# Optimization experiments

Hardware: AMD Instinct MI355X
Metric: run time of the kernel (lower is better)

## Reference

```python
import jax, jax.numpy as jnp
import numpy as np

B, L_ENC, L_DEC, PRED_LEN = 16, 720, 144, 96
D_MODEL, N_HEADS, D_FF, M_FEAT = 512, 8, 2048, 256
ENC_IN, DEC_IN, C_OUT, MARK = 7, 7, 7, 4
E_LAYERS = 2
DH = D_MODEL // N_HEADS


def _orf(m, d, seed):
    # Gaussian orthogonal random features (FAVOR+), scaling=0 (chi-norm rows).
    rng = np.random.default_rng(seed)
    blocks = [np.linalg.qr(rng.standard_normal((d, d)))[0].T for _ in range(m // d)]
    mat = np.concatenate(blocks, 0)  # [m, d]
    mult = np.linalg.norm(rng.standard_normal((m, d)), axis=1)
    return jnp.asarray(mult[:, None] * mat, dtype=jnp.float32)

PROJ_ENC = [_orf(M_FEAT, DH, s) for s in range(E_LAYERS)]
PROJ_DEC_SELF = _orf(M_FEAT, DH, 10)
PROJ_DEC_CROSS = _orf(M_FEAT, DH, 11)


def _pos_emb(n, d):
    pos = np.arange(n, dtype=np.float32)[:, None]
    div = np.exp(np.arange(0, d, 2, dtype=np.float32) * (-np.log(10000.0) / d))
    pe = np.zeros((n, d), dtype=np.float32)
    pe[:, 0::2] = np.sin(pos * div)
    pe[:, 1::2] = np.cos(pos * div)
    return jnp.asarray(pe)

PE_ENC = _pos_emb(L_ENC, D_MODEL)
PE_DEC = _pos_emb(L_DEC, D_MODEL)


def layer_norm(x, g, b):
    mu = x.mean(-1, keepdims=True)
    var = ((x - mu) ** 2).mean(-1, keepdims=True)
    return (x - mu) / jnp.sqrt(var + 1e-5) * g + b


def feature_map(x, proj, is_query):
    # FAVOR+ positive softmax kernel. x: [b,h,n,dh], proj: [m,dh]
    norm = DH ** -0.25
    xd = jnp.einsum('bhnd,md->bhnm', x * norm, proj)
    diag = (x ** 2).sum(-1) * (0.5 * norm * norm)  # [b,h,n]
    if is_query:
        stab = jax.lax.stop_gradient(xd.max(axis=-1, keepdims=True))
    else:
        stab = jax.lax.stop_gradient(xd.max(axis=(-1, -2), keepdims=True))
    return (M_FEAT ** -0.5) * (jnp.exp(xd - diag[..., None] - stab) + 1e-4)


def noncausal_attn(q, k, v):
    kv = jnp.einsum('bhnm,bhnd->bhmd', k, v)
    d_inv = 1.0 / jnp.einsum('bhnm,bhm->bhn', q, k.sum(2))
    return jnp.einsum('bhnm,bhmd,bhn->bhnd', q, kv, d_inv)


def causal_attn(q, k, v):
    # prefix-sum linear attention; carry S [b,h,m,dh], s [b,h,m]
    b, h, n, m = q.shape
    dh = v.shape[-1]

    def step(carry, qkv):
        S, s = carry
        qn, kn, vn = qkv
        S = S + kn[..., None] * vn[..., None, :]
        s = s + kn
        num = jnp.einsum('bhm,bhmd->bhd', qn, S)
        den = jnp.einsum('bhm,bhm->bh', qn, s)
        return (S, s), num / (den[..., None] + 1e-6)

    init = (jnp.zeros((b, h, m, dh), q.dtype), jnp.zeros((b, h, m), q.dtype))
    _, out = jax.lax.scan(step, init, (jnp.moveaxis(q, 2, 0), jnp.moveaxis(k, 2, 0), jnp.moveaxis(v, 2, 0)))
    return jnp.moveaxis(out, 0, 2)


def attention(x, ctx, Wq, Wk, Wv, Wo, bo, proj, causal):
    b, n, _ = x.shape
    nc = ctx.shape[1]
    q = (x @ Wq).reshape(b, n, N_HEADS, DH).transpose(0, 2, 1, 3)
    k = (ctx @ Wk).reshape(b, nc, N_HEADS, DH).transpose(0, 2, 1, 3)
    v = (ctx @ Wv).reshape(b, nc, N_HEADS, DH).transpose(0, 2, 1, 3)
    qp = feature_map(q, proj, True)
    kp = feature_map(k, proj, False)
    o = causal_attn(qp, kp, v) if causal else noncausal_attn(qp, kp, v)
    o = o.transpose(0, 2, 1, 3).reshape(b, n, D_MODEL)
    return o @ Wo + bo


def embed(x, mark, conv_w, time_w, pe):
    # TokenEmbedding: circular conv1d k=3 (no bias) + fixed sinusoidal PE + timeF linear
    xp = jnp.concatenate([x[:, -1:], x, x[:, :1]], axis=1)
    tok = (jnp.einsum('blc,cd->bld', xp[:, :-2], conv_w[0])
           + jnp.einsum('blc,cd->bld', xp[:, 1:-1], conv_w[1])
           + jnp.einsum('blc,cd->bld', xp[:, 2:], conv_w[2]))
    return tok + pe[None] + mark @ time_w


def _forward(x_enc, x_mark_enc, x_dec, x_mark_dec,
             emb_conv_enc, emb_time_enc, emb_conv_dec, emb_time_dec,
             enc_Wq, enc_Wk, enc_Wv, enc_Wo, enc_bo,
             enc_ff1, enc_b1, enc_ff2, enc_b2, enc_ln_g, enc_ln_b, enc_fg, enc_fb,
             dec_sWq, dec_sWk, dec_sWv, dec_sWo, dec_sbo,
             dec_cWq, dec_cWk, dec_cWv, dec_cWo, dec_cbo,
             dec_ff1, dec_b1, dec_ff2, dec_b2, dec_ln_g, dec_ln_b, dec_fg, dec_fb,
             proj_w, proj_b):
    gelu = lambda t: jax.nn.gelu(t, approximate=False)
    # RevIN-style instance normalization (means detached, as in the torch code)
    means = jax.lax.stop_gradient(x_enc.mean(1, keepdims=True))
    xc = x_enc - means
    stdev = jnp.sqrt(xc.var(1, keepdims=True) + 1e-5)
    xe = xc / stdev

    enc = embed(xe, x_mark_enc, emb_conv_enc, emb_time_enc, PE_ENC)
    for i in range(E_LAYERS):
        a = attention(enc, enc, enc_Wq[i], enc_Wk[i], enc_Wv[i], enc_Wo[i], enc_bo[i], PROJ_ENC[i], False)
        x1 = layer_norm(enc + a, enc_ln_g[i, 0], enc_ln_b[i, 0])
        y = gelu(x1 @ enc_ff1[i] + enc_b1[i]) @ enc_ff2[i] + enc_b2[i]
        enc = layer_norm(x1 + y, enc_ln_g[i, 1], enc_ln_b[i, 1])
    enc = layer_norm(enc, enc_fg, enc_fb)

    dec = embed(x_dec, x_mark_dec, emb_conv_dec, emb_time_dec, PE_DEC)
    a = attention(dec, dec, dec_sWq, dec_sWk, dec_sWv, dec_sWo, dec_sbo, PROJ_DEC_SELF, True)
    x1 = layer_norm(dec + a, dec_ln_g[0], dec_ln_b[0])
    c = attention(x1, enc, dec_cWq, dec_cWk, dec_cWv, dec_cWo, dec_cbo, PROJ_DEC_CROSS, False)
    x2 = layer_norm(x1 + c, dec_ln_g[1], dec_ln_b[1])
    y = gelu(x2 @ dec_ff1 + dec_b1) @ dec_ff2 + dec_b2
    dec = layer_norm(x2 + y, dec_ln_g[2], dec_ln_b[2])
    dec = layer_norm(dec, dec_fg, dec_fb)
    out = dec @ proj_w + proj_b  # [B, L_DEC, C_OUT]

    out = out * stdev[:, 0][:, None, :] + means[:, 0][:, None, :]
    return out[:, -PRED_LEN:, :]


def setup_inputs():
    ks = iter(jax.random.split(jax.random.key(0), 48))

    def rn(shape, scale=1.0):
        return jax.random.normal(next(ks), shape, dtype=jnp.float32) * scale

    w = 0.02
    E, D, F = E_LAYERS, D_MODEL, D_FF
    return {
        'x_enc': rn((B, L_ENC, ENC_IN)),
        'x_mark_enc': rn((B, L_ENC, MARK)),
        'x_dec': rn((B, L_DEC, DEC_IN)),
        'x_mark_dec': rn((B, L_DEC, MARK)),
        'emb_conv_enc': rn((3, ENC_IN, D), 0.1),
        'emb_time_enc': rn((MARK, D), w),
        'emb_conv_dec': rn((3, DEC_IN, D), 0.1),
        'emb_time_dec': rn((MARK, D), w),
        'enc_Wq': rn((E, D, D), w), 'enc_Wk': rn((E, D, D), w),
        'enc_Wv': rn((E, D, D), w), 'enc_Wo': rn((E, D, D), w),
        'enc_bo': jnp.zeros((E, D), jnp.float32),
        'enc_ff1': rn((E, D, F), w), 'enc_b1': jnp.zeros((E, F), jnp.float32),
        'enc_ff2': rn((E, F, D), w), 'enc_b2': jnp.zeros((E, D), jnp.float32),
        'enc_ln_g': jnp.ones((E, 2, D), jnp.float32), 'enc_ln_b': jnp.zeros((E, 2, D), jnp.float32),
        'enc_fg': jnp.ones((D,), jnp.float32), 'enc_fb': jnp.zeros((D,), jnp.float32),
        'dec_sWq': rn((D, D), w), 'dec_sWk': rn((D, D), w), 'dec_sWv': rn((D, D), w), 'dec_sWo': rn((D, D), w),
        'dec_sbo': jnp.zeros((D,), jnp.float32),
        'dec_cWq': rn((D, D), w), 'dec_cWk': rn((D, D), w), 'dec_cWv': rn((D, D), w), 'dec_cWo': rn((D, D), w),
        'dec_cbo': jnp.zeros((D,), jnp.float32),
        'dec_ff1': rn((D, F), w), 'dec_b1': jnp.zeros((F,), jnp.float32),
        'dec_ff2': rn((F, D), w), 'dec_b2': jnp.zeros((D,), jnp.float32),
        'dec_ln_g': jnp.ones((3, D), jnp.float32), 'dec_ln_b': jnp.zeros((3, D), jnp.float32),
        'dec_fg': jnp.ones((D,), jnp.float32), 'dec_fb': jnp.zeros((D,), jnp.float32),
        'proj_w': rn((D, C_OUT), w), 'proj_b': jnp.zeros((C_OUT,), jnp.float32),
    }


def reference(x_enc, x_mark_enc, x_dec, x_mark_dec,
              emb_conv_enc, emb_time_enc, emb_conv_dec, emb_time_dec,
              enc_Wq, enc_Wk, enc_Wv, enc_Wo, enc_bo,
              enc_ff1, enc_b1, enc_ff2, enc_b2, enc_ln_g, enc_ln_b, enc_fg, enc_fb,
              dec_sWq, dec_sWk, dec_sWv, dec_sWo, dec_sbo,
              dec_cWq, dec_cWk, dec_cWv, dec_cWo, dec_cbo,
              dec_ff1, dec_b1, dec_ff2, dec_b2, dec_ln_g, dec_ln_b, dec_fg, dec_fb,
              proj_w, proj_b):
    return _forward(x_enc, x_mark_enc, x_dec, x_mark_dec,
                    emb_conv_enc, emb_time_enc, emb_conv_dec, emb_time_dec,
                    enc_Wq, enc_Wk, enc_Wv, enc_Wo, enc_bo,
                    enc_ff1, enc_b1, enc_ff2, enc_b2, enc_ln_g, enc_ln_b, enc_fg, enc_fb,
                    dec_sWq, dec_sWk, dec_sWv, dec_sWo, dec_sbo,
                    dec_cWq, dec_cWk, dec_cWv, dec_cWo, dec_cbo,
                    dec_ff1, dec_b1, dec_ff2, dec_b2, dec_ln_g, dec_ln_b, dec_fg, dec_fb,
                    proj_w, proj_b)
```

## Files before the change

### kernel.cpp

```cpp
#include <hip/hip_runtime.h>
#include <math.h>
#include <string.h>

#define BB    16
#define LEc   720
#define LDc   144
#define PREDc 96
#define DMc   512
#define NHc   8
#define DHc   64
#define MFc   256
#define FFc   2048
#define NEc   (BB*LEc)
#define NDc   (BB*LDc)
#define BHc   (BB*NHc)
#define KSn   ((size_t)BHc*MFc)

typedef unsigned int u32;
typedef unsigned short u16;
typedef unsigned long long u64;
typedef unsigned __int128 u128;

typedef short bfx8 __attribute__((ext_vector_type(8)));
typedef float fx4  __attribute__((ext_vector_type(4)));
// ... 193 lines not shown
                                             int K, int N){
  __shared__ float t[32][33];
  int kb = blockIdx.x*32, nb = blockIdx.y*32;
  int tx = threadIdx.x & 31, ty = threadIdx.x >> 5;
  #pragma unroll
  for (int p=0;p<4;p++)
    t[ty + p*8][tx] = W[(size_t)(kb + ty + p*8)*N + nb + tx];
  __syncthreads();
  #pragma unroll
  for (int p=0;p<4;p++)
    WT[(size_t)(nb + ty + p*8)*K + kb + tx] = f2bf(t[tx][ty + p*8]);
}

__global__ __launch_bounds__(64) void k_meanstd(const float* __restrict__ x,
                                                float* __restrict__ means, float* __restrict__ stdev){
  int bc = blockIdx.x; int b = bc/7, c = bc%7;
  int t = threadIdx.x;
  float s=0;
  for (int l=t; l<LEc; l+=64) s += x[((size_t)b*LEc+l)*7 + c];
  for (int o=32;o;o>>=1) s += __shfl_down(s,o);
  s = __shfl(s,0);
  float mu = s / (float)LEc;
  float v=0;
  for (int l=t; l<LEc; l+=64){ float d = x[((size_t)b*LEc+l)*7+c]-mu; v += d*d; }
  for (int o=32;o;o>>=1) v += __shfl_down(v,o);
  if (t==0){ means[bc]=mu; stdev[bc]=sqrtf(v/(float)LEc + 1e-5f); }
}

__global__ __launch_bounds__(256) void k_embed(const float* __restrict__ x, const float* __restrict__ mark,
    const float* __restrict__ convw, const float* __restrict__ timew, const float* __restrict__ pe,
    const float* __restrict__ means, const float* __restrict__ stdev,
    int L, int donorm, float* __restrict__ outp)
{
  size_t idx = (size_t)blockIdx.x*256 + threadIdx.x;
  size_t total = (size_t)BB*L*DMc;
  if (idx >= total) return;
  int d = (int)(idx % DMc); size_t bl = idx / DMc; int l = (int)(bl % L); int b = (int)(bl / L);
  int lm = (l==0)? L-1 : l-1;
  int lp = (l==L-1)? 0 : l+1;
  float acc = pe[(size_t)l*DMc + d];
  const float* xb = x + (size_t)b*L*7;
  #pragma unroll
  for (int c=0;c<7;c++){
    float v0 = xb[(size_t)lm*7+c], v1 = xb[(size_t)l*7+c], v2 = xb[(size_t)lp*7+c];
    if (donorm){
      float mu = means[b*7+c], sd = stdev[b*7+c];
      v0=(v0-mu)/sd; v1=(v1-mu)/sd; v2=(v2-mu)/sd;
    }
    acc += v0*convw[(0*7+c)*DMc+d] + v1*convw[(1*7+c)*DMc+d] + v2*convw[(2*7+c)*DMc+d];
  }
  const float* mb = mark + ((size_t)b*L + l)*4;
  #pragma unroll
  for (int t=0;t<4;t++) acc += mb[t]*timew[t*DMc+d];
  outp[idx] = acc;
}

template<int A_BF16, int OUT_BF16, int GELU>
__global__ __launch_bounds__(256) void k_gemm_mfma(
    const void* __restrict__ Ap, const u16* __restrict__ WT,
    const float* __restrict__ bias, void* __restrict__ Cp,
    int M, int N, int K)
{
  __shared__ u16 As[128][40];
  __shared__ u16 Bs[128][40];
  int nb = N >> 7;
  int bid = blockIdx.x;
  int nwg = gridDim.x;
  if (!(nwg & 7)) bid = ((bid & 7) * (nwg >> 3)) + (bid >> 3);
  int bx = bid % nb, by = bid / nb;
  int row0 = by << 7, col0 = bx << 7;
  int tid = threadIdx.x;
  int wid = tid >> 6, lane = tid & 63;
  int wr = (wid >> 1) * 64, wc = (wid & 1) * 64;
  int l15 = lane & 15, lg = lane >> 4;
  fx4 acc[4][4];
  #pragma unroll
  for (int i=0;i<4;i++)
    #pragma unroll
    for (int j=0;j<4;j++)
      #pragma unroll
      for (int r=0;r<4;r++) acc[i][j][r] = 0.f;

  for (int k0 = 0; k0 < K; k0 += 32){
    if (A_BF16){
      const u16* A = (const u16*)Ap;
      #pragma unroll
      for (int p=0;p<2;p++){
        int idx = tid + (p<<8);
        int r = idx >> 2, kq = (idx & 3) << 3;
        *(bfx8*)&As[r][kq] = *(const bfx8*)(A + (size_t)(row0+r)*K + k0 + kq);
      }
    } else {
      const float* A = (const float*)Ap;
      #pragma unroll
      for (int p=0;p<4;p++){
        int idx = tid + (p<<8);
        int r = idx >> 3, kq = (idx & 7) << 2;
        float4 v = *(const float4*)(A + (size_t)(row0+r)*K + k0 + kq);
        u32 lo = (u32)f2bf(v.x) | ((u32)f2bf(v.y) << 16);
        u32 hi = (u32)f2bf(v.z) | ((u32)f2bf(v.w) << 16);
        *(u32*)&As[r][kq]   = lo;
        *(u32*)&As[r][kq+2] = hi;
      }
    }
    #pragma unroll
    for (int p=0;p<2;p++){
      int idx = tid + (p<<8);
      int c = idx >> 2, kq = (idx & 3) << 3;
      *(bfx8*)&Bs[c][kq] = *(const bfx8*)(WT + (size_t)(col0+c)*K + k0 + kq);
    }
    __syncthreads();
    int kg = lg << 3;
    bfx8 af[4], bf[4];
    #pragma unroll
    for (int i=0;i<4;i++) af[i] = *(const bfx8*)&As[wr + i*16 + l15][kg];
    #pragma unroll
    for (int j=0;j<4;j++) bf[j] = *(const bfx8*)&Bs[wc + j*16 + l15][kg];
    #pragma unroll
    for (int i=0;i<4;i++)
      #pragma unroll
      for (int j=0;j<4;j++)
        acc[i][j] = __builtin_amdgcn_mfma_f32_16x16x32_bf16(af[i], bf[j], acc[i][j], 0, 0, 0);
    __syncthreads();
  }
  #pragma unroll
  for (int j=0;j<4;j++){
    int col = col0 + wc + j*16 + l15;
    float bv = bias ? bias[col] : 0.f;
    #pragma unroll
    for (int i=0;i<4;i++){
      #pragma unroll
      for (int r=0;r<4;r++){
        int row = row0 + wr + i*16 + (lg<<2) + r;
        float v = acc[i][j][r] + bv;
        if (GELU) v = 0.5f*v*(1.0f + erff(v*0.7071067811865475f));
        if (OUT_BF16) ((u16*)Cp)[(size_t)row*N + col] = f2bf(v);
        else          ((float*)Cp)[(size_t)row*N + col] = v;
      }
    }
  }
}

static inline void gemm_bf(const void* A, const u16* WT, const float* bias, void* C,
                           int M, int N, int K, int abf, int obf, int gelu, hipStream_t st){
  dim3 g((N/128)*(M/128));
  if (abf && obf && gelu)  k_gemm_mfma<1,1,1><<<g,256,0,st>>>(A,WT,bias,C,M,N,K);
  else if (abf && obf)     k_gemm_mfma<1,1,0><<<g,256,0,st>>>(A,WT,bias,C,M,N,K);
  else if (abf)            k_gemm_mfma<1,0,0><<<g,256,0,st>>>(A,WT,bias,C,M,N,K);
  else if (gelu)           k_gemm_mfma<0,1,1><<<g,256,0,st>>>(A,WT,bias,C,M,N,K);
  else if (obf)            k_gemm_mfma<0,1,0><<<g,256,0,st>>>(A,WT,bias,C,M,N,K);
  else                     k_gemm_mfma<0,0,0><<<g,256,0,st>>>(A,WT,bias,C,M,N,K);
}

__global__ __launch_bounds__(256) void k_rowmax_mfma(const u16* __restrict__ Kb,
    const u16* __restrict__ projbf, float* __restrict__ rowmax, int n)
{
  int ntile = n >> 4;
  int rt = blockIdx.x % ntile, bh = blockIdx.x / ntile;
  int b = bh >> 3, h = bh & 7;
  int row0 = rt << 4;
  int tid = threadIdx.x, w = tid >> 6, lane = tid & 63;
  int l15 = lane & 15, lg = lane >> 4;
  __shared__ u16 qs[16][72];
  __shared__ float xds[16][264];
  __shared__ float red[16][16];
  for (int i = tid; i < 16*16; i += 256){
    int r = i >> 4, dq = (i & 15)*4;
    *(u16x4*)&qs[r][dq] = *(const u16x4*)(Kb + ((size_t)b*n + row0 + r)*DMc + h*64 + dq);
  }
  __syncthreads();
  #pragma unroll
  for (int mt=0; mt<4; mt++){
    int m16 = (w*4+mt)*16;
    fx4 a2 = {0.f,0.f,0.f,0.f};
    #pragma unroll
    for (int ks=0; ks<2; ks++){
      bfx8 af = *(const bfx8*)&qs[l15][ks*32 + lg*8];
      bfx8 bf = *(const bfx8*)(projbf + (size_t)(m16+l15)*64 + ks*32 + lg*8);
      a2 = __builtin_amdgcn_mfma_f32_16x16x32_bf16(af, bf, a2, 0, 0, 0);
    }
    #pragma unroll
    for (int r=0;r<4;r++)
      xds[lg*4+r][m16+l15] = a2[r];
  }
  __syncthreads();
  { int r = tid >> 4, s = tid & 15;
    float mx = -1e30f;
    #pragma unroll
    for (int j=0;j<16;j++) mx = fmaxf(mx, xds[r][s*16+j]);
    red[r][s] = mx; }
  __syncthreads();
  if (tid < 16){
    float mx = -1e30f;
    #pragma unroll
    for (int j=0;j<16;j++) mx = fmaxf(mx, red[tid][j]);
    rowmax[(size_t)bh*n + row0 + tid] = mx * 0.35355339059327373f;
  }
}

__global__ __launch_bounds__(256) void k_stab(const float* __restrict__ rowmax, float* __restrict__ stab, int n){
  int bh = blockIdx.x; int tid = threadIdx.x;
  float mx = -1e30f;
  for (int i=tid;i<n;i+=256) mx = fmaxf(mx, rowmax[(size_t)bh*n+i]);
  __shared__ float red[4];
  for (int o=32;o;o>>=1) mx = fmaxf(mx, __shfl_xor(mx,o));
  if ((tid&63)==0) red[tid>>6]=mx;
  __syncthreads();
  if (tid==0) stab[bh] = fmaxf(fmaxf(red[0],red[1]),fmaxf(red[2],red[3]));
}

__global__ __launch_bounds__(256) void k_vtr(const u16* __restrict__ Vb, u16* __restrict__ Vt, int n){
  int nt = n >> 4;
  int blk = blockIdx.x; int t16 = blk % nt; int bh = blk / nt;
  int b = bh >> 3, h = bh & 7;
  int n0 = t16 << 4;
  int t = threadIdx.x;
  __shared__ u16 vt[16][72];
  { int r = t >> 4, d0 = (t & 15) * 4;
    *(u16x4*)&vt[r][d0] = *(const u16x4*)(Vb + ((size_t)b*n + n0 + r)*DMc + h*64 + d0); }
  __syncthreads();
  { int d = t >> 2, j = t & 3;
    u16x4 o;
    o.x = vt[j*4+0][d]; o.y = vt[j*4+1][d]; o.z = vt[j*4+2][d]; o.w = vt[j*4+3][d];
    *(u16x4*)(Vt + ((size_t)bh*64 + d)*(size_t)n + n0 + j*4) = o; }
}

__global__ __launch_bounds__(256) void k_kvfull(const u16* __restrict__ Kb,
    const u16* __restrict__ Vt, const u16* __restrict__ projbf, const float* __restrict__ stab,
    u16* __restrict__ KVT, float* __restrict__ KS, int n)
{
  int bh = blockIdx.x >> 1; int dh = (blockIdx.x & 1) * 32;
  int b = bh >> 3, h = bh & 7;
  int tid = threadIdx.x, w = tid >> 6, lane = tid & 63;
  int l15 = lane & 15, lg = lane >> 4;
  float sb = stab[bh];
  __shared__ u16 ksb[32][72];
  __shared__ u16 kpT[256][40];
  __shared__ u16 vsb[32][40];
  __shared__ float dgs[32];
  fx4 kv[2][4];
  #pragma unroll
  for (int i=0;i<2;i++)
    #pragma unroll
    for (int j=0;j<4;j++)
      #pragma unroll
      for (int r=0;r<4;r++) kv[i][j][r] = 0.f;
  float ksl[4] = {0.f,0.f,0.f,0.f};
  int nchunks = (n + 31) >> 5;
  for (int c=0; c<nchunks; c++){
    int n0 = c << 5;
    for (int i = tid; i < 32*16; i += 256){
      int r = i >> 4, dq = (i & 15) * 4;
      u16x4 v = {0,0,0,0};
      if (n0 + r < n) v = *(const u16x4*)(Kb + ((size_t)b*n + n0 + r)*DMc + h*64 + dq);
      *(u16x4*)&ksb[r][dq] = v;
    }
    for (int i = tid; i < 32*8; i += 256){
      int r = i >> 3, nq4 = (i & 7) * 4;
      u16x4 v = {0,0,0,0};
      const u16* src = Vt + ((size_t)bh*64 + dh + r)*(size_t)n + n0 + nq4;
      if (n0 + nq4 + 3 < n) v = *(const u16x4*)src;
      else { for (int j=0;j<4;j++) if (n0+nq4+j < n) v[j] = src[j]; }
      *(u16x4*)&vsb[r][nq4] = v;
    }
    __syncthreads();
    {
      int r = tid >> 3, j = tid & 7;
      float dg = 0;
      #pragma unroll
      for (int q=0;q<8;q++){ float kd = bf2f(ksb[r][j*8+q]); dg = fmaf(kd,kd,dg); }
      dg += __shfl_down(dg,4); dg += __shfl_down(dg,2); dg += __shfl_down(dg,1);
      if (j == 0) dgs[r] = dg * 0.0625f;
    }
    __syncthreads();
    #pragma unroll
    for (int mt=0; mt<4; mt++){
      int m16 = (w*4 + mt)*16;
      #pragma unroll
      for (int nt=0; nt<2; nt++){
        fx4 a2 = {0.f,0.f,0.f,0.f};
        #pragma unroll
        for (int ks=0; ks<2; ks++){
          bfx8 af = *(const bfx8*)&ksb[nt*16 + l15][ks*32 + lg*8];
          bfx8 bf = *(const bfx8*)(projbf + (size_t)(m16 + l15)*64 + ks*32 + lg*8);
          a2 = __builtin_amdgcn_mfma_f32_16x16x32_bf16(af, bf, a2, 0, 0, 0);
        }
        #pragma unroll
        for (int r=0;r<4;r++){
          int nn = nt*16 + lg*4 + r;
          float kp = 0.f;
          if (n0 + nn < n)
            kp = (__expf(a2[r]*0.35355339059327373f - dgs[nn] - sb) + 1e-4f) * 0.0625f;
          ksl[mt] += kp;
          kpT[m16 + l15][nn] = f2bf(kp);
        }
      }
    }
    __syncthreads();
    #pragma unroll
    for (int dt=0; dt<2; dt++){
      #pragma unroll
      for (int mt=0; mt<4; mt++){
        bfx8 af = *(const bfx8*)&vsb[dt*16 + l15][lg*8];
        bfx8 bf = *(const bfx8*)&kpT[(w*4+mt)*16 + l15][lg*8];
        kv[dt][mt] = __builtin_amdgcn_mfma_f32_16x16x32_bf16(af, bf, kv[dt][mt], 0, 0, 0);
      }
    }
    __syncthreads();
  }
  if (dh == 0){
    #pragma unroll
    for (int mt=0; mt<4; mt++){
      float v = ksl[mt];
      v += __shfl_xor(v, 16);
      v += __shfl_xor(v, 32);
      if (lg == 0) KS[(size_t)bh*MFc + (w*4+mt)*16 + l15] = v;
    }
  }
  #pragma unroll
  for (int dt=0; dt<2; dt++)
    #pragma unroll
    for (int mt=0; mt<4; mt++)
      #pragma unroll
      for (int r=0;r<4;r++){
        int d = dh + dt*16 + lg*4 + r;
        int m = (w*4+mt)*16 + l15;
        KVT[((size_t)bh*64 + d)*MFc + m] = f2bf(kv[dt][mt][r]);
      }
}

__global__ __launch_bounds__(256) void k_attn_mfma(const u16* __restrict__ Qb,
    const u16* __restrict__ projbf, const u16* __restrict__ KVT, const float* __restrict__ KS,
    u16* __restrict__ O, int nq)
{
  int ntile = nq >> 4;
  int rt = blockIdx.x % ntile, bh = blockIdx.x / ntile;
  int b = bh >> 3, h = bh & 7;
  int row0 = rt << 4;
  int tid = threadIdx.x, w = tid >> 6, lane = tid & 63;
  int l15 = lane & 15, lg = lane >> 4;
  __shared__ u16 qs[16][72];
  __shared__ float xds[16][264];
  __shared__ u16 qpl[16][264];
  __shared__ float dgs[16], mxs[16], dns[16];
  __shared__ float red[16][16];
  __shared__ float kss[256];
  for (int i = tid; i < 16*16; i += 256){
    int r = i >> 4, dq = (i & 15)*4;
    *(u16x4*)&qs[r][dq] = *(const u16x4*)(Qb + ((size_t)b*nq + row0 + r)*DMc + h*64 + dq);
  }
  kss[tid] = KS[(size_t)bh*MFc + tid];
  __syncthreads();
  if (tid < 16){
    float dg = 0;
    #pragma unroll 16
    for (int d=0;d<64;d++){ float q = bf2f(qs[tid][d]); dg = fmaf(q,q,dg); }
    dgs[tid] = dg * 0.0625f;
  }
  #pragma unroll
  for (int mt=0; mt<4; mt++){
    int m16 = (w*4+mt)*16;
    fx4 a2 = {0.f,0.f,0.f,0.f};
    #pragma unroll
    for (int ks=0; ks<2; ks++){
      bfx8 af = *(const bfx8*)&qs[l15][ks*32 + lg*8];
      bfx8 bf = *(const bfx8*)(projbf + (size_t)(m16+l15)*64 + ks*32 + lg*8);
      a2 = __builtin_amdgcn_mfma_f32_16x16x32_bf16(af, bf, a2, 0, 0, 0);
    }
    #pragma unroll
    for (int r=0;r<4;r++)
      xds[lg*4+r][m16+l15] = a2[r]*0.35355339059327373f;
  }
  __syncthreads();
  { int r = tid >> 4, s = tid & 15;
    float mx = -1e30f;
    #pragma unroll
    for (int j=0;j<16;j++) mx = fmaxf(mx, xds[r][s*16+j]);
    red[r][s] = mx; }
  __syncthreads();
  if (tid < 16){
    float mx = -1e30f;
    #pragma unroll
    for (int j=0;j<16;j++) mx = fmaxf(mx, red[tid][j]);
    mxs[tid] = mx;
  }
  __syncthreads();
  { int r = tid >> 4, s = tid & 15;
    float dg = dgs[r], mx = mxs[r], pd = 0;
    #pragma unroll
    for (int j=0;j<16;j++){
      int m = s*16+j;
      float v = (__expf(xds[r][m] - dg - mx) + 1e-4f)*0.0625f;
      qpl[r][m] = f2bf(v);
      pd = fmaf(v, kss[m], pd);
    }
    red[r][s] = pd; }
  __syncthreads();
  if (tid < 16){
    float s = 0;
    #pragma unroll
    for (int j=0;j<16;j++) s += red[tid][j];
    dns[tid] = 1.0f / s;
  }
  __syncthreads();
  fx4 a2 = {0.f,0.f,0.f,0.f};
  #pragma unroll
  for (int ks=0; ks<8; ks++){
    bfx8 af = *(const bfx8*)&qpl[l15][ks*32 + lg*8];
    bfx8 bf = *(const bfx8*)(KVT + ((size_t)bh*64 + w*16 + l15)*MFc + ks*32 + lg*8);
    a2 = __builtin_amdgcn_mfma_f32_16x16x32_bf16(af, bf, a2, 0, 0, 0);
  }
  #pragma unroll
  for (int r=0;r<4;r++){
    int row = lg*4 + r;
    O[((size_t)b*nq + row0 + row)*DMc + h*64 + w*16 + l15] = f2bf(a2[r]*dns[row]);
  }
}

template<int ISQ>
__global__ __launch_bounds__(256) void k_fmap_mfma(const u16* __restrict__ Xb,
    const u16* __restrict__ projbf, const float* __restrict__ stab,
    u16* __restrict__ P, int n)
{
  int ntile = n >> 4;
  int rt = blockIdx.x % ntile, bh = blockIdx.x / ntile;
  int b = bh >> 3, h = bh & 7;
  int row0 = rt << 4;
  int tid = threadIdx.x, w = tid >> 6, lane = tid & 63;
  int l15 = lane & 15, lg = lane >> 4;
  __shared__ u16 qs[16][72];
  __shared__ float xds[16][264];
  __shared__ float dgs[16], mxs[16];
  __shared__ float red[16][16];
  for (int i = tid; i < 16*16; i += 256){
    int r = i >> 4, dq = (i & 15)*4;
    *(u16x4*)&qs[r][dq] = *(const u16x4*)(Xb + ((size_t)b*n + row0 + r)*DMc + h*64 + dq);
  }
  __syncthreads();
  if (tid < 16){
    float dg = 0;
    #pragma unroll 16
    for (int d=0;d<64;d++){ float q = bf2f(qs[tid][d]); dg = fmaf(q,q,dg); }
    dgs[tid] = dg * 0.0625f;
  }
  #pragma unroll
  for (int mt=0; mt<4; mt++){
    int m16 = (w*4+mt)*16;
    fx4 a2 = {0.f,0.f,0.f,0.f};
    #pragma unroll
    for (int ks=0; ks<2; ks++){
      bfx8 af = *(const bfx8*)&qs[l15][ks*32 + lg*8];
      bfx8 bf = *(const bfx8*)(projbf + (size_t)(m16+l15)*64 + ks*32 + lg*8);
      a2 = __builtin_amdgcn_mfma_f32_16x16x32_bf16(af, bf, a2, 0, 0, 0);
    }
    #pragma unroll
    for (int r=0;r<4;r++)
      xds[lg*4+r][m16+l15] = a2[r]*0.35355339059327373f;
  }
  __syncthreads();
  if (ISQ){
    { int r = tid >> 4, s = tid & 15;
      float mx = -1e30f;
      #pragma unroll
      for (int j=0;j<16;j++) mx = fmaxf(mx, xds[r][s*16+j]);
      red[r][s] = mx; }
    __syncthreads();
    if (tid < 16){
      float mx = -1e30f;
      #pragma unroll
      for (int j=0;j<16;j++) mx = fmaxf(mx, red[tid][j]);
      mxs[tid] = mx;
    }
    __syncthreads();
  }
  { int r = tid >> 4, s = tid & 15;
    float sv = ISQ ? mxs[r] : stab[bh];
    float dg = dgs[r];
    u16* dst = P + ((size_t)bh*n + row0 + r)*MFc;
    #pragma unroll
// ... 148 lines not shown
  #pragma unroll
  for (int c=0;c<7;c++){
    float s = acc[c];
    for (int o=32;o;o>>=1) s += __shfl_xor(s,o);
    if (t==0)
      outp[((size_t)b*PREDc + lo)*7 + c] = (s + pb[c]) * stdev[b*7+c] + means[b*7+c];
  }
}

extern "C" void kernel_launch(void* const* d_in, const int* in_sizes, int n_in,
                              void* d_out, int out_size, void* d_ws, size_t ws_size,
                              hipStream_t stream)
{
  (void)in_sizes; (void)n_in;
  const float* x_enc        = (const float*)d_in[0];
  const float* x_mark_enc   = (const float*)d_in[1];
  const float* x_dec        = (const float*)d_in[2];
  const float* x_mark_dec   = (const float*)d_in[3];
  const float* emb_conv_enc = (const float*)d_in[4];
  const float* emb_time_enc = (const float*)d_in[5];
  const float* emb_conv_dec = (const float*)d_in[6];
  const float* emb_time_dec = (const float*)d_in[7];
  const float* enc_Wq = (const float*)d_in[8];
  const float* enc_Wk = (const float*)d_in[9];
  const float* enc_Wv = (const float*)d_in[10];
  const float* enc_Wo = (const float*)d_in[11];
  const float* enc_bo = (const float*)d_in[12];
  const float* enc_ff1 = (const float*)d_in[13];
  const float* enc_b1  = (const float*)d_in[14];
  const float* enc_ff2 = (const float*)d_in[15];
  const float* enc_b2  = (const float*)d_in[16];
  const float* enc_ln_g = (const float*)d_in[17];
  const float* enc_ln_b = (const float*)d_in[18];
  const float* enc_fg = (const float*)d_in[19];
  const float* enc_fb = (const float*)d_in[20];
  const float* dec_sWq = (const float*)d_in[21];
  const float* dec_sWk = (const float*)d_in[22];
  const float* dec_sWv = (const float*)d_in[23];
  const float* dec_sWo = (const float*)d_in[24];
  const float* dec_sbo = (const float*)d_in[25];
  const float* dec_cWq = (const float*)d_in[26];
  const float* dec_cWk = (const float*)d_in[27];
  const float* dec_cWv = (const float*)d_in[28];
  const float* dec_cWo = (const float*)d_in[29];
  const float* dec_cbo = (const float*)d_in[30];
  const float* dec_ff1 = (const float*)d_in[31];
  const float* dec_b1  = (const float*)d_in[32];
  const float* dec_ff2 = (const float*)d_in[33];
  const float* dec_b2  = (const float*)d_in[34];
  const float* dec_ln_g = (const float*)d_in[35];
  const float* dec_ln_b = (const float*)d_in[36];
  const float* dec_fg = (const float*)d_in[37];
  const float* dec_fb = (const float*)d_in[38];
  const float* proj_w = (const float*)d_in[39];
  const float* proj_b = (const float*)d_in[40];
  float* outp = (float*)d_out;
  float* W = (float*)d_ws;

  size_t o = 0;
  #define ALLOCF(nm, n) size_t nm = o; o += (((size_t)(n)) + 63) & ~(size_t)63;
  ALLOCF(o_proj, 4*MFc*DHc)
  ALLOCF(o_projbf, 2*MFc*DHc)
  ALLOCF(o_means, BB*7)
  ALLOCF(o_std,   BB*7)
  ALLOCF(o_rmE, (size_t)BHc*LEc)
  ALLOCF(o_rmD, (size_t)BHc*LDc)
  ALLOCF(o_stab, BHc)
  ALLOCF(o_KS, KSn)
  ALLOCF(o_PE, (size_t)LEc*DMc)
  ALLOCF(o_Dx1, (size_t)NDc*DMc)
  ALLOCF(o_WT, 5242880)
  ALLOCF(o_Xb, (size_t)NEc*DMc)
  ALLOCF(o_X1, (size_t)NEc*DMc)
  ALLOCF(o_U,  11796480)
  #undef ALLOCF
  size_t needed_bytes = o * sizeof(float);
  if (ws_size < needed_bytes){
    k_zero<<<(out_size+255)/256, 256, 0, stream>>>(outp, out_size);
    return;
  }

  float* Xb  = W + o_Xb;
  float* X1  = W + o_X1;
  float* KS  = W + o_KS;
  float* PE  = W + o_PE;
  float* rmE = W + o_rmE;
  float* rmD = W + o_rmD;
  float* stb = W + o_stab;
  u16*  WTb = (u16*)(W + o_WT);
  u16*  Uh  = (u16*)(W + o_U);
  u16*  PJB = (u16*)(W + o_projbf);

  const size_t NEu = (size_t)NEc*DMc;
  const size_t NDu = (size_t)NDc*DMc;
  u16* Tq = Uh;            u16* Tk = Uh + NEu;
  u16* Tv = Uh + 2*NEu;    u16* Oe = Uh + 3*NEu;
  u16* FFb = Uh;
  u16*   VtU  = (u16*)X1;
  u16*   KVTu = (u16*)(X1 + 2949120);
  u16*   x1bf   = (u16*)X1;
  u16*   attnbf = (u16*)X1 + NEu;
  u16* dTq = Uh;           u16* dTk = Uh + NDu;
  u16* dTv = Uh + 2*NDu;   u16* dOd = Uh + 3*NDu;
  u16* PQb = Uh + 4*NDu;
  u16* PKb = PQb + (size_t)BHc*LDc*MFc;
  u16* VtD = PKb + (size_t)BHc*LDc*MFc;
  u16* cTk = Uh;           u16* cTv = Uh + NEu;
  u16* dTq2 = Uh + 2*NEu;  u16* cOd = Uh + 2*NEu + NDu;
  u16* dFF = Uh;
  float* DX  = X1 + 0*NDu;
  float* Da  = X1 + 1*NDu;
  float* Dx2 = X1 + 2*NDu;
  float* Dy  = X1 + 3*NDu;
  u16* dAttnbf = (u16*)Da;
  u16* Dx1bf   = (u16*)(W + o_Dx1);
  u16* Dx2bf   = (u16*)Dx2;

  static float h_proj[4*MFc*DHc];
  build_all_proj(h_proj);
  hipMemcpyAsync(W + o_proj, h_proj, sizeof(h_proj), hipMemcpyHostToDevice, stream);
  k_projbf<<<(4*MFc*DHc)/256, 256, 0, stream>>>(W + o_proj, PJB, 4*MFc*DHc);
  const u16* pb_enc0  = PJB + 0*MFc*DHc;
  const u16* pb_enc1  = PJB + 1*MFc*DHc;
  const u16* pb_self  = PJB + 2*MFc*DHc;
  const u16* pb_cross = PJB + 3*MFc*DHc;

  k_petab<<<(LEc*DMc)/256, 256, 0, stream>>>(PE);

  size_t wto = 0;
  auto xpose = [&](const float* Wsrc, int K, int N) -> const u16* {
    u16* dst = WTb + wto; wto += (size_t)K*N;
    k_wtr<<<dim3(K/32, N/32), 256, 0, stream>>>(Wsrc, dst, K, N);
    return dst;
  };
  const u16 *wQ[2], *wK[2], *wV[2], *wO[2], *wF1[2], *wF2[2];
  for (int i=0;i<2;i++){
    wQ[i]  = xpose(enc_Wq + (size_t)i*DMc*DMc, DMc, DMc);
    wK[i]  = xpose(enc_Wk + (size_t)i*DMc*DMc, DMc, DMc);
    wV[i]  = xpose(enc_Wv + (size_t)i*DMc*DMc, DMc, DMc);
    wO[i]  = xpose(enc_Wo + (size_t)i*DMc*DMc, DMc, DMc);
    wF1[i] = xpose(enc_ff1 + (size_t)i*DMc*FFc, DMc, FFc);
    wF2[i] = xpose(enc_ff2 + (size_t)i*FFc*DMc, FFc, DMc);
  }
  const u16* wsQ = xpose(dec_sWq, DMc, DMc);
  const u16* wsK = xpose(dec_sWk, DMc, DMc);
  const u16* wsV = xpose(dec_sWv, DMc, DMc);
  const u16* wsO = xpose(dec_sWo, DMc, DMc);
  const u16* wcQ = xpose(dec_cWq, DMc, DMc);
  const u16* wcK = xpose(dec_cWk, DMc, DMc);
  const u16* wcV = xpose(dec_cWv, DMc, DMc);
  const u16* wcO = xpose(dec_cWo, DMc, DMc);
  const u16* wdF1 = xpose(dec_ff1, DMc, FFc);
  const u16* wdF2 = xpose(dec_ff2, FFc, DMc);

  auto kv_chain = [&](const u16* Kbuf, const u16* Vbuf, const u16* pjb){
    k_rowmax_mfma<<<BHc*(LEc/16), 256, 0, stream>>>(Kbuf, pjb, rmE, LEc);
    k_stab<<<BHc, 256, 0, stream>>>(rmE, stb, LEc);
    k_vtr<<<BHc*(LEc/16), 256, 0, stream>>>(Vbuf, VtU, LEc);
    k_kvfull<<<BHc*2, 256, 0, stream>>>(Kbuf, VtU, pjb, stb, KVTu, KS, LEc);
  };

  k_meanstd<<<BB*7, 64, 0, stream>>>(x_enc, W+o_means, W+o_std);
  k_embed<<<(BB*LEc*DMc)/256, 256, 0, stream>>>(x_enc, x_mark_enc, emb_conv_enc, emb_time_enc,
                                                PE, W+o_means, W+o_std, LEc, 1, Xb);

  for (int i=0;i<2;i++){
    const float* bo = enc_bo + (size_t)i*DMc;
    const float* b1 = enc_b1  + (size_t)i*FFc;
    const float* b2 = enc_b2  + (size_t)i*DMc;
    const float* g0 = enc_ln_g + (size_t)(i*2+0)*DMc;
    const float* e0 = enc_ln_b + (size_t)(i*2+0)*DMc;
    const float* g1 = enc_ln_g + (size_t)(i*2+1)*DMc;
    const float* e1 = enc_ln_b + (size_t)(i*2+1)*DMc;
    const u16*   pjb = (i==0) ? pb_enc0 : pb_enc1;

    gemm_bf(Xb, wQ[i], nullptr, Tq, NEc, DMc, DMc, 0,1,0, stream);
    gemm_bf(Xb, wK[i], nullptr, Tk, NEc, DMc, DMc, 0,1,0, stream);
    gemm_bf(Xb, wV[i], nullptr, Tv, NEc, DMc, DMc, 0,1,0, stream);
    kv_chain(Tk, Tv, pjb);
    k_attn_mfma<<<BHc*(LEc/16), 256, 0, stream>>>(Tq, pjb, KVTu, KS, Oe, LEc);
    gemm_bf(Oe, wO[i], bo, attnbf, NEc, DMc, DMc, 1,1,0, stream);
    k_ln<1,0,1><<<NEc, 128, 0, stream>>>(attnbf, Xb, g0, e0, x1bf);
    gemm_bf(x1bf, wF1[i], b1, FFb, NEc, FFc, DMc, 1,1,1, stream);
    gemm_bf(FFb, wF2[i], b2, Xb, NEc, DMc, FFc, 1,0,0, stream);
    k_ln<0,1,0><<<NEc, 128, 0, stream>>>(Xb, x1bf, g1, e1, Xb);
  }
  k_ln<0,0,0><<<NEc, 128, 0, stream>>>(Xb, nullptr, enc_fg, enc_fb, Xb);

  k_embed<<<(BB*LDc*DMc)/256, 256, 0, stream>>>(x_dec, x_mark_dec, emb_conv_dec, emb_time_dec,
                                                PE, W+o_means, W+o_std, LDc, 0, DX);
  gemm_bf(DX, wsQ, nullptr, dTq, NDc, DMc, DMc, 0,1,0, stream);
  gemm_bf(DX, wsK, nullptr, dTk, NDc, DMc, DMc, 0,1,0, stream);
  gemm_bf(DX, wsV, nullptr, dTv, NDc, DMc, DMc, 0,1,0, stream);
  k_rowmax_mfma<<<BHc*(LDc/16), 256, 0, stream>>>(dTk, pb_self, rmD, LDc);
  k_stab<<<BHc, 256, 0, stream>>>(rmD, stb, LDc);
  k_fmap_mfma<1><<<BHc*(LDc/16), 256, 0, stream>>>(dTq, pb_self, nullptr, PQb, LDc);
  k_fmap_mfma<0><<<BHc*(LDc/16), 256, 0, stream>>>(dTk, pb_self, stb, PKb, LDc);
  k_vtr<<<BHc*(LDc/16), 256, 0, stream>>>(dTv, VtD, LDc);
  k_causal_mfma<<<BHc*(LDc/16), 256, 0, stream>>>(PQb, PKb, VtD, dOd, LDc);
  gemm_bf(dOd, wsO, dec_sbo, dAttnbf, NDc, DMc, DMc, 1,1,0, stream);
  k_ln<1,0,1><<<NDc, 128, 0, stream>>>(dAttnbf, DX, dec_ln_g + 0*DMc, dec_ln_b + 0*DMc, Dx1bf);

  gemm_bf(Dx1bf, wcQ, nullptr, dTq2, NDc, DMc, DMc, 1,1,0, stream);
  gemm_bf(Xb,  wcK, nullptr, cTk,  NEc, DMc, DMc, 0,1,0, stream);
  gemm_bf(Xb,  wcV, nullptr, cTv,  NEc, DMc, DMc, 0,1,0, stream);
  kv_chain(cTk, cTv, pb_cross);
  k_attn_mfma<<<BHc*(LDc/16), 256, 0, stream>>>(dTq2, pb_cross, KVTu, KS, cOd, LDc);
  gemm_bf(cOd, wcO, dec_cbo, Da, NDc, DMc, DMc, 1,0,0, stream);
  k_ln<0,1,1><<<NDc, 128, 0, stream>>>(Da, Dx1bf, dec_ln_g + 1*DMc, dec_ln_b + 1*DMc, Dx2bf);

  gemm_bf(Dx2bf, wdF1, dec_b1, dFF, NDc, FFc, DMc, 1,1,1, stream);
  gemm_bf(dFF, wdF2, dec_b2, Dy, NDc, DMc, FFc, 1,0,0, stream);
  k_ln<0,1,0><<<NDc, 128, 0, stream>>>(Dy, Dx2bf, dec_ln_g + 2*DMc, dec_ln_b + 2*DMc, Da);
  k_ln<0,0,0><<<NDc, 128, 0, stream>>>(Da, nullptr, dec_fg, dec_fb, Da);
  k_final<<<BB*PREDc, 64, 0, stream>>>(Da, proj_w, proj_b, W+o_means, W+o_std, outp);
}
```

Before: 1.343 ms.

## Fuse Q/K/V projections into one GEMM and split KV reduction across feature halves

Replaces the three separate Q, K and V projection GEMMs (two for cross-attention K and V) with one kernel. It treats the transposed weights as one concatenated matrix and routes each 512-column segment to its own output buffer, so the fp32 activation is read and converted once and fewer kernels are launched. It also splits k_kvfull over two 128-feature halves, doubling the block count to raise parallelism. The fusion relies on the transposed weight buffers for Q, K and V being contiguous in memory.

```diff
diff --git a/kernel.cpp b/kernel.cpp
--- a/kernel.cpp
+++ b/kernel.cpp
@@ -369,6 +369,81 @@
   else                     k_gemm_mfma<0,0,0><<<g,256,0,st>>>(A,WT,bias,C,M,N,K);
 }
 
+template<int NSEG>
+__global__ __launch_bounds__(256) void k_gemm_qkv(
+    const float* __restrict__ Ap, const u16* __restrict__ WT,
+    u16* __restrict__ C0, u16* __restrict__ C1, u16* __restrict__ C2,
+    int M, int K)
+{
+  const int N = NSEG*512;
+  __shared__ u16 As[128][40];
+  __shared__ u16 Bs[128][40];
+  int nb = N >> 7;
+  int bid = blockIdx.x;
+  int nwg = gridDim.x;
+  if (!(nwg & 7)) bid = ((bid & 7) * (nwg >> 3)) + (bid >> 3);
+  int bx = bid % nb, by = bid / nb;
+  int row0 = by << 7, col0 = bx << 7;
+  int tid = threadIdx.x;
+  int wid = tid >> 6, lane = tid & 63;
+  int wr = (wid >> 1) * 64, wc = (wid & 1) * 64;
+  int l15 = lane & 15, lg = lane >> 4;
+  fx4 acc[4][4];
+  #pragma unroll
+  for (int i=0;i<4;i++)
+    #pragma unroll
+    for (int j=0;j<4;j++)
+      #pragma unroll
+      for (int r=0;r<4;r++) acc[i][j][r] = 0.f;
+
+  for (int k0 = 0; k0 < K; k0 += 32){
+    #pragma unroll
+    for (int p=0;p<4;p++){
+      int idx = tid + (p<<8);
+      int r = idx >> 3, kq = (idx & 7) << 2;
+      float4 v = *(const float4*)(Ap + (size_t)(row0+r)*K + k0 + kq);
+      u32 lo = (u32)f2bf(v.x) | ((u32)f2bf(v.y) << 16);
+      u32 hi = (u32)f2bf(v.z) | ((u32)f2bf(v.w) << 16);
+      *(u32*)&As[r][kq]   = lo;
+      *(u32*)&As[r][kq+2] = hi;
+    }
+    #pragma unroll
+    for (int p=0;p<2;p++){
+      int idx = tid + (p<<8);
+      int c = idx >> 2, kq = (idx & 3) << 3;
+      *(bfx8*)&Bs[c][kq] = *(const bfx8*)(WT + (size_t)(col0+c)*K + k0 + kq);
+    }
+    __syncthreads();
+    int kg = lg << 3;
+    bfx8 af[4], bf[4];
+    #pragma unroll
+    for (int i=0;i<4;i++) af[i] = *(const bfx8*)&As[wr + i*16 + l15][kg];
+    #pragma unroll
+    for (int j=0;j<4;j++) bf[j] = *(const bfx8*)&Bs[wc + j*16 + l15][kg];
+    #pragma unroll
+    for (int i=0;i<4;i++)
+      #pragma unroll
+      for (int j=0;j<4;j++)
+        acc[i][j] = __builtin_amdgcn_mfma_f32_16x16x32_bf16(af[i], bf[j], acc[i][j], 0, 0, 0);
+    __syncthreads();
+  }
+  int seg = col0 >> 9;
+  u16* Cs = (seg==0) ? C0 : (seg==1) ? C1 : C2;
+  int cb = col0 - (seg << 9);
+  #pragma unroll
+  for (int j=0;j<4;j++){
+    int col = cb + wc + j*16 + l15;
+    #pragma unroll
+    for (int i=0;i<4;i++){
+      #pragma unroll
+      for (int r=0;r<4;r++){
+        int row = row0 + wr + i*16 + (lg<<2) + r;
+        Cs[(size_t)row*512 + col] = f2bf(acc[i][j][r]);
+      }
+    }
+  }
+}
+
 __global__ __launch_bounds__(256) void k_rowmax_mfma(const u16* __restrict__ Kb,
     const u16* __restrict__ projbf, float* __restrict__ rowmax, int n)
 {
@@ -446,23 +521,27 @@
     const u16* __restrict__ Vt, const u16* __restrict__ projbf, const float* __restrict__ stab,
     u16* __restrict__ KVT, float* __restrict__ KS, int n)
 {
-  int bh = blockIdx.x >> 1; int dh = (blockIdx.x & 1) * 32;
+  int mh = blockIdx.x & 1;
+  int rest = blockIdx.x >> 1;
+  int dh = (rest & 1) * 32;
+  int bh = rest >> 1;
   int b = bh >> 3, h = bh & 7;
   int tid = threadIdx.x, w = tid >> 6, lane = tid & 63;
   int l15 = lane & 15, lg = lane >> 4;
+  int m0 = mh * 128;
   float sb = stab[bh];
   __shared__ u16 ksb[32][72];
-  __shared__ u16 kpT[256][40];
+  __shared__ u16 kpT[128][40];
   __shared__ u16 vsb[32][40];
   __shared__ float dgs[32];
-  fx4 kv[2][4];
+  fx4 kv[2][2];
   #pragma unroll
   for (int i=0;i<2;i++)
     #pragma unroll
-    for (int j=0;j<4;j++)
+    for (int j=0;j<2;j++)
       #pragma unroll
       for (int r=0;r<4;r++) kv[i][j][r] = 0.f;
-  float ksl[4] = {0.f,0.f,0.f,0.f};
+  float ksl[2] = {0.f,0.f};
   int nchunks = (n + 31) >> 5;
   for (int c=0; c<nchunks; c++){
     int n0 = c << 5;
@@ -491,15 +570,16 @@
     }
     __syncthreads();
     #pragma unroll
-    for (int mt=0; mt<4; mt++){
-      int m16 = (w*4 + mt)*16;
+    for (int mt=0; mt<2; mt++){
+      int ml = (w*2 + mt)*16;
+      int mg = m0 + ml;
       #pragma unroll
       for (int nt=0; nt<2; nt++){
         fx4 a2 = {0.f,0.f,0.f,0.f};
         #pragma unroll
         for (int ks=0; ks<2; ks++){
           bfx8 af = *(const bfx8*)&ksb[nt*16 + l15][ks*32 + lg*8];
-          bfx8 bf = *(const bfx8*)(projbf + (size_t)(m16 + l15)*64 + ks*32 + lg*8);
+          bfx8 bf = *(const bfx8*)(projbf + (size_t)(mg + l15)*64 + ks*32 + lg*8);
           a2 = __builtin_amdgcn_mfma_f32_16x16x32_bf16(af, bf, a2, 0, 0, 0);
         }
         #pragma unroll
@@ -509,7 +589,7 @@
           if (n0 + nn < n)
             kp = (__expf(a2[r]*0.35355339059327373f - dgs[nn] - sb) + 1e-4f) * 0.0625f;
           ksl[mt] += kp;
-          kpT[m16 + l15][nn] = f2bf(kp);
+          kpT[ml + l15][nn] = f2bf(kp);
         }
       }
     }
@@ -517,9 +597,9 @@
     #pragma unroll
     for (int dt=0; dt<2; dt++){
       #pragma unroll
-      for (int mt=0; mt<4; mt++){
+      for (int mt=0; mt<2; mt++){
         bfx8 af = *(const bfx8*)&vsb[dt*16 + l15][lg*8];
-        bfx8 bf = *(const bfx8*)&kpT[(w*4+mt)*16 + l15][lg*8];
+        bfx8 bf = *(const bfx8*)&kpT[(w*2+mt)*16 + l15][lg*8];
         kv[dt][mt] = __builtin_amdgcn_mfma_f32_16x16x32_bf16(af, bf, kv[dt][mt], 0, 0, 0);
       }
     }
@@ -527,21 +607,21 @@
   }
   if (dh == 0){
     #pragma unroll
-    for (int mt=0; mt<4; mt++){
+    for (int mt=0; mt<2; mt++){
       float v = ksl[mt];
       v += __shfl_xor(v, 16);
       v += __shfl_xor(v, 32);
-      if (lg == 0) KS[(size_t)bh*MFc + (w*4+mt)*16 + l15] = v;
+      if (lg == 0) KS[(size_t)bh*MFc + m0 + (w*2+mt)*16 + l15] = v;
     }
   }
   #pragma unroll
   for (int dt=0; dt<2; dt++)
     #pragma unroll
-    for (int mt=0; mt<4; mt++)
+    for (int mt=0; mt<2; mt++)
       #pragma unroll
       for (int r=0;r<4;r++){
         int d = dh + dt*16 + lg*4 + r;
-        int m = (w*4+mt)*16 + l15;
+        int m = m0 + (w*2+mt)*16 + l15;
         KVT[((size_t)bh*64 + d)*MFc + m] = f2bf(kv[dt][mt][r]);
       }
 }
@@ -996,12 +1076,13 @@
   const u16* wcO = xpose(dec_cWo, DMc, DMc);
   const u16* wdF1 = xpose(dec_ff1, DMc, FFc);
   const u16* wdF2 = xpose(dec_ff2, FFc, DMc);
+  (void)wK; (void)wV; (void)wsK; (void)wsV; (void)wcV;
 
   auto kv_chain = [&](const u16* Kbuf, const u16* Vbuf, const u16* pjb){
     k_rowmax_mfma<<<BHc*(LEc/16), 256, 0, stream>>>(Kbuf, pjb, rmE, LEc);
     k_stab<<<BHc, 256, 0, stream>>>(rmE, stb, LEc);
     k_vtr<<<BHc*(LEc/16), 256, 0, stream>>>(Vbuf, VtU, LEc);
-    k_kvfull<<<BHc*2, 256, 0, stream>>>(Kbuf, VtU, pjb, stb, KVTu, KS, LEc);
+    k_kvfull<<<BHc*2*2, 256, 0, stream>>>(Kbuf, VtU, pjb, stb, KVTu, KS, LEc);
   };
 
   k_meanstd<<<BB*7, 64, 0, stream>>>(x_enc, W+o_means, W+o_std);
@@ -1018,9 +1099,7 @@
     const float* e1 = enc_ln_b + (size_t)(i*2+1)*DMc;
     const u16*   pjb = (i==0) ? pb_enc0 : pb_enc1;
 
-    gemm_bf(Xb, wQ[i], nullptr, Tq, NEc, DMc, DMc, 0,1,0, stream);
-    gemm_bf(Xb, wK[i], nullptr, Tk, NEc, DMc, DMc, 0,1,0, stream);
-    gemm_bf(Xb, wV[i], nullptr, Tv, NEc, DMc, DMc, 0,1,0, stream);
+    k_gemm_qkv<3><<<dim3((1536/128)*(NEc/128)), 256, 0, stream>>>(Xb, wQ[i], Tq, Tk, Tv, NEc, DMc);
     kv_chain(Tk, Tv, pjb);
     k_attn_mfma<<<BHc*(LEc/16), 256, 0, stream>>>(Tq, pjb, KVTu, KS, Oe, LEc);
     gemm_bf(Oe, wO[i], bo, attnbf, NEc, DMc, DMc, 1,1,0, stream);
@@ -1033,9 +1112,7 @@
 
   k_embed<<<(BB*LDc*DMc)/256, 256, 0, stream>>>(x_dec, x_mark_dec, emb_conv_dec, emb_time_dec,
                                                 PE, W+o_means, W+o_std, LDc, 0, DX);
-  gemm_bf(DX, wsQ, nullptr, dTq, NDc, DMc, DMc, 0,1,0, stream);
-  gemm_bf(DX, wsK, nullptr, dTk, NDc, DMc, DMc, 0,1,0, stream);
-  gemm_bf(DX, wsV, nullptr, dTv, NDc, DMc, DMc, 0,1,0, stream);
+  k_gemm_qkv<3><<<dim3((1536/128)*(NDc/128)), 256, 0, stream>>>(DX, wsQ, dTq, dTk, dTv, NDc, DMc);
   k_rowmax_mfma<<<BHc*(LDc/16), 256, 0, stream>>>(dTk, pb_self, rmD, LDc);
   k_stab<<<BHc, 256, 0, stream>>>(rmD, stb, LDc);
   k_fmap_mfma<1><<<BHc*(LDc/16), 256, 0, stream>>>(dTq, pb_self, nullptr, PQb, LDc);
@@ -1046,8 +1123,7 @@
   k_ln<1,0,1><<<NDc, 128, 0, stream>>>(dAttnbf, DX, dec_ln_g + 0*DMc, dec_ln_b + 0*DMc, Dx1bf);
 
   gemm_bf(Dx1bf, wcQ, nullptr, dTq2, NDc, DMc, DMc, 1,1,0, stream);
-  gemm_bf(Xb,  wcK, nullptr, cTk,  NEc, DMc, DMc, 0,1,0, stream);
-  gemm_bf(Xb,  wcV, nullptr, cTv,  NEc, DMc, DMc, 0,1,0, stream);
+  k_gemm_qkv<2><<<dim3((1024/128)*(NEc/128)), 256, 0, stream>>>(Xb, wcK, cTk, cTv, nullptr, NEc, DMc);
   kv_chain(cTk, cTv, pb_cross);
   k_attn_mfma<<<BHc*(LDc/16), 256, 0, stream>>>(dTq2, pb_cross, KVTu, KS, cOd, LDc);
   gemm_bf(cOd, wcO, dec_cbo, Da, NDc, DMc, DMc, 1,0,0, stream);
```

After: 3.747 ms. +178.9%, slower.
